# Performance work log

Measured on AMD Instinct MI355X. Metric: run time of the kernel, lower is better.

## Reference

```python
import jax, jax.numpy as jnp
import numpy as np

VOCAB, EMB, B, L, H, OUT = 100000, 300, 2048, 200, 128, 20

def setup_inputs() -> dict:
    key = jax.random.key(0)
    ks = jax.random.split(key, 7)
    x = jax.random.randint(ks[0], (B, L), 0, VOCAB, dtype=jnp.int64 if jax.config.read('jax_enable_x64') else jnp.int32)
    lengths = jax.random.randint(ks[1], (B,), 1, L + 1, dtype=x.dtype)  # avoid zero length
    emb_table = jax.random.normal(ks[2], (VOCAB, EMB), dtype=jnp.float32)
    W1 = jax.random.normal(ks[3], (EMB, H), dtype=jnp.float32) * (1.0 / np.sqrt(EMB))
    b1 = jax.random.normal(ks[4], (H,), dtype=jnp.float32) * 0.01
    W2 = jax.random.normal(ks[5], (H, OUT), dtype=jnp.float32) * (1.0 / np.sqrt(H))
    b2 = jax.random.normal(ks[6], (OUT,), dtype=jnp.float32) * 0.01
    return {"x": x, "lengths": lengths, "emb_table": emb_table,
            "W1": W1, "b1": b1, "W2": W2, "b2": b2}

def reference(x, lengths, emb_table, W1, b1, W2, b2):
    # embedding lookup: [B, L, EMB]
    emb = emb_table[x]
    # faithful to original: sum over FULL sequence, divide by per-sample length
    rep = emb.sum(axis=1) / lengths.astype(emb.dtype)[:, None]  # [B, EMB]
    h = jax.nn.relu(rep @ W1 + b1)                              # [B, H]
    logits = h @ W2 + b2                                        # [B, OUT]
    return logits
```

## Files before the change

kernel.cpp:

```cpp
#include <hip/hip_runtime.h>

#define BB   2048
#define LL   200
#define EMB  300
#define HH   128
#define OUTD 20
#define NSRT 256
#define RPW  (LL / 4)

__global__ __launch_bounds__(256) void fused_dnn(
    const int*   __restrict__ x,
    const int*   __restrict__ lengths,
    const float* __restrict__ table,
    const float* __restrict__ W1,
    const float* __restrict__ b1,
    const float* __restrict__ W2,
    const float* __restrict__ b2,
    float*       __restrict__ out)
{
    __shared__ int    idx_s[NSRT];
    __shared__ float4 part_s[4][76];
    __shared__ float  rep_s[EMB];
    __shared__ float  h_part[2][HH];
    __shared__ float  h_s[HH];

    const int b    = blockIdx.x;
    const int t    = threadIdx.x;
    const int w    = t >> 6;
    const int lane = t & 63;

    idx_s[t] = (t < LL) ? x[b * LL + t] : 0x7FFFFFFF;
    __syncthreads();

    #pragma unroll
    for (int k = 2; k <= NSRT; k <<= 1) {
        #pragma unroll
        for (int j = k >> 1; j > 0; j >>= 1) {
            const int ixj = t ^ j;
            if (ixj > t) {
                const int a0 = idx_s[t];
                const int a1 = idx_s[ixj];
                const bool up = ((t & k) == 0);
                if ((a0 > a1) == up) { idx_s[t] = a1; idx_s[ixj] = a0; }
            }
            __syncthreads();
        }
    }

    const int myidx = (lane < RPW) ? idx_s[w + 4 * lane] : 0;

    float4 acc_a = make_float4(0.f, 0.f, 0.f, 0.f);
    float4 acc_b = make_float4(0.f, 0.f, 0.f, 0.f);
    const bool hasb = (lane < (EMB / 4 - 64));

    #pragma unroll 5
    for (int i = 0; i < RPW; ++i) {
        const int ridx = __builtin_amdgcn_readlane(myidx, i);
        const float4* row = (const float4*)(table + (size_t)ridx * EMB);
        float4 va = row[lane];
        acc_a.x += va.x; acc_a.y += va.y; acc_a.z += va.z; acc_a.w += va.w;
        if (hasb) {
            float4 vb = row[64 + lane];
            acc_b.x += vb.x; acc_b.y += vb.y; acc_b.z += vb.z; acc_b.w += vb.w;
        }
    }

    part_s[w][lane] = acc_a;
    if (hasb) part_s[w][64 + lane] = acc_b;
    __syncthreads();

    const float inv_len = 1.0f / (float)lengths[b];
    const float* ps = (const float*)part_s;
    {
        float s = ps[t] + ps[304 + t] + ps[608 + t] + ps[912 + t];
        rep_s[t] = s * inv_len;
    }
    if (t < (EMB - 256)) {
        int c = 256 + t;
        float s = ps[c] + ps[304 + c] + ps[608 + c] + ps[912 + c];
        rep_s[c] = s * inv_len;
    }
    __syncthreads();

    {
        const int half = t >> 7;
        const int col  = t & 127;
        float hacc = (half == 0) ? b1[col] : 0.0f;
        const int k0 = half * (EMB / 2);
        #pragma unroll 5
        for (int k = k0; k < k0 + EMB / 2; ++k)
            hacc = fmaf(rep_s[k], W1[k * HH + col], hacc);
        h_part[half][col] = hacc;
    }
    __syncthreads();
    if (t < HH)
        h_s[t] = fmaxf(h_part[0][t] + h_part[1][t], 0.0f);
    __syncthreads();

    if (t < OUTD) {
        float oacc = b2[t];
        #pragma unroll
        for (int k = 0; k < HH; ++k)
            oacc = fmaf(h_s[k], W2[k * OUTD + t], oacc);
        out[b * OUTD + t] = oacc;
    }
}

extern "C" void kernel_launch(void* const* d_in, const int* in_sizes, int n_in,
                              void* d_out, int out_size, void* d_ws, size_t ws_size,
                              hipStream_t stream) {
    const int*   x       = (const int*)  d_in[0];
    const int*   lengths = (const int*)  d_in[1];
    const float* table   = (const float*)d_in[2];
    const float* W1      = (const float*)d_in[3];
    const float* b1      = (const float*)d_in[4];
    const float* W2      = (const float*)d_in[5];
    const float* b2      = (const float*)d_in[6];
    float*       out     = (float*)d_out;

    fused_dnn<<<BB, 256, 0, stream>>>(x, lengths, table, W1, b1, W2, b2, out);
}
```

Measured before the change: 241.6 us.

## Software-pipeline embedding row gathers and repack tail columns across lanes

The main gather loop now keeps a rolling buffer of six row loads in flight, so several independent global loads are outstanding per wave instead of one at a time. The 11 leftover float4 columns per row used to be handled by a predicated second load on 11 of 64 lanes. They are now spread across 55 lanes, each covering 5 row subsets, and gathered in a separate double-buffered pass. This raises memory-level parallelism and lane utilisation for the tail. In exchange it costs more registers, an extra shared buffer, and a 20-term reduction for the tail columns.

```diff
diff --git a/kernel.cpp b/kernel.cpp
--- a/kernel.cpp
+++ b/kernel.cpp
@@ -7,6 +7,7 @@
 #define OUTD 20
 #define NSRT 256
 #define RPW  (LL / 4)
+#define DP   6
 
 __global__ __launch_bounds__(256) void fused_dnn(
     const int*   __restrict__ x,
@@ -19,7 +20,8 @@
     float*       __restrict__ out)
 {
     __shared__ int    idx_s[NSRT];
-    __shared__ float4 part_s[4][76];
+    __shared__ float4 part_s[4][64];
+    __shared__ float4 tails[4][56];
     __shared__ float  rep_s[EMB];
     __shared__ float  h_part[2][HH];
     __shared__ float  h_s[HH];
@@ -50,35 +52,66 @@
     const int myidx = (lane < RPW) ? idx_s[w + 4 * lane] : 0;
 
     float4 acc_a = make_float4(0.f, 0.f, 0.f, 0.f);
-    float4 acc_b = make_float4(0.f, 0.f, 0.f, 0.f);
-    const bool hasb = (lane < (EMB / 4 - 64));
-
-    #pragma unroll 5
-    for (int i = 0; i < RPW; ++i) {
-        const int ridx = __builtin_amdgcn_readlane(myidx, i);
-        const float4* row = (const float4*)(table + (size_t)ridx * EMB);
-        float4 va = row[lane];
-        acc_a.x += va.x; acc_a.y += va.y; acc_a.z += va.z; acc_a.w += va.w;
-        if (hasb) {
-            float4 vb = row[64 + lane];
-            acc_b.x += vb.x; acc_b.y += vb.y; acc_b.z += vb.z; acc_b.w += vb.w;
+    {
+        float4 buf[DP];
+        #pragma unroll
+        for (int u = 0; u < DP; ++u) {
+            const int r = __builtin_amdgcn_readlane(myidx, u);
+            buf[u] = ((const float4*)(table + (size_t)r * EMB))[lane];
+        }
+        #pragma unroll
+        for (int i = 0; i < RPW; ++i) {
+            const float4 v = buf[i % DP];
+            if (i + DP < RPW) {
+                const int r = __builtin_amdgcn_readlane(myidx, i + DP);
+                buf[i % DP] = ((const float4*)(table + (size_t)r * EMB))[lane];
+            }
+            acc_a.x += v.x; acc_a.y += v.y; acc_a.z += v.z; acc_a.w += v.w;
         }
     }
+    part_s[w][lane] = acc_a;
 
-    part_s[w][lane] = acc_a;
-    if (hasb) part_s[w][64 + lane] = acc_b;
+    float4 acc_t = make_float4(0.f, 0.f, 0.f, 0.f);
+    {
+        const int g     = lane % 11;
+        const int sub   = lane / 11;
+        const int sub_c = (lane < 55) ? sub : 4;
+        float4 tbuf[2];
+        #pragma unroll
+        for (int u = 0; u < 2; ++u) {
+            const int r = idx_s[w + 4 * (u * 5 + sub_c)];
+            tbuf[u] = ((const float4*)(table + (size_t)r * EMB))[64 + g];
+        }
+        #pragma unroll
+        for (int i = 0; i < RPW / 5; ++i) {
+            const float4 v = tbuf[i & 1];
+            if (i + 2 < RPW / 5) {
+                const int r = idx_s[w + 4 * ((i + 2) * 5 + sub_c)];
+                tbuf[i & 1] = ((const float4*)(table + (size_t)r * EMB))[64 + g];
+            }
+            acc_t.x += v.x; acc_t.y += v.y; acc_t.z += v.z; acc_t.w += v.w;
+        }
+        tails[w][sub_c * 11 + g] = acc_t;
+    }
     __syncthreads();
 
     const float inv_len = 1.0f / (float)lengths[b];
-    const float* ps = (const float*)part_s;
     {
-        float s = ps[t] + ps[304 + t] + ps[608 + t] + ps[912 + t];
+        const float* ps = (const float*)part_s;
+        float s = ps[t] + ps[256 + t] + ps[512 + t] + ps[768 + t];
         rep_s[t] = s * inv_len;
     }
     if (t < (EMB - 256)) {
-        int c = 256 + t;
-        float s = ps[c] + ps[304 + c] + ps[608 + c] + ps[912 + c];
-        rep_s[c] = s * inv_len;
+        const int g4   = t >> 2;
+        const int comp = t & 3;
+        const float* tf = (const float*)tails;
+        float s = 0.f;
+        #pragma unroll
+        for (int ww = 0; ww < 4; ++ww)
+            #pragma unroll
+            for (int sb = 0; sb < 5; ++sb)
+                s += tf[(ww * 56 + sb * 11 + g4) * 4 + comp];
+        rep_s[256 + t] = s * inv_len;
     }
     __syncthreads();
 
```

Measured after the change: 244.6 us. No clear change (+1.3%).

## Quantize embedding table to int8 per row before gathering

Applied to the files above, without the earlier changes.

Adds a pre-pass kernel that quantizes the full fp32 embedding table into int8 with a per-row scale, stored in workspace. The fused kernel then gathers 300-byte int8 rows and dequantizes them with an FMA, instead of gathering 1200-byte fp32 rows. The aim is to cut the random-gather traffic, which dominates the cost, at the price of a full streaming pass over the table on every call and lossy quantization error in the sums. It falls back to the fp32 path when the workspace is too small.

```diff
diff --git a/kernel.cpp b/kernel.cpp
--- a/kernel.cpp
+++ b/kernel.cpp
@@ -1,14 +1,166 @@
 #include <hip/hip_runtime.h>
 
-#define BB   2048
-#define LL   200
-#define EMB  300
-#define HH   128
-#define OUTD 20
-#define NSRT 256
-#define RPW  (LL / 4)
-
-__global__ __launch_bounds__(256) void fused_dnn(
+#define BB    2048
+#define LL    200
+#define EMB   300
+#define HH    128
+#define OUTD  20
+#define NSRT  256
+#define VOCAB 100000
+#define RPW   (LL / 4)
+
+#define QTAB_BYTES (VOCAB * 300)
+#define SC_OFF     QTAB_BYTES
+#define WS_NEED    (QTAB_BYTES + VOCAB * 4)
+
+__global__ __launch_bounds__(256) void quant_table(
+    const float*   __restrict__ table,
+    unsigned char* __restrict__ qt,
+    float*         __restrict__ sc)
+{
+    const int row  = blockIdx.x * 4 + (threadIdx.x >> 6);
+    const int lane = threadIdx.x & 63;
+    const bool hb  = (lane < (EMB / 4 - 64));
+
+    const float4* rp = (const float4*)(table + (size_t)row * EMB);
+    float4 fa = rp[lane];
+    float4 fb = make_float4(0.f, 0.f, 0.f, 0.f);
+    if (hb) fb = rp[64 + lane];
+
+    float m = fmaxf(fmaxf(fabsf(fa.x), fabsf(fa.y)), fmaxf(fabsf(fa.z), fabsf(fa.w)));
+    m = fmaxf(m, fmaxf(fmaxf(fabsf(fb.x), fabsf(fb.y)), fmaxf(fabsf(fb.z), fabsf(fb.w))));
+    #pragma unroll
+    for (int o = 32; o >= 1; o >>= 1)
+        m = fmaxf(m, __shfl_xor(m, o, 64));
+
+    const float inv   = (m > 0.f) ? 127.0f / m : 0.0f;
+    const float scale = (m > 0.f) ? m / 127.0f : 0.0f;
+
+    unsigned int* qrow = (unsigned int*)(qt + (size_t)row * 300);
+    {
+        const unsigned int q0 = (unsigned int)((int)rintf(fa.x * inv) & 0xff);
+        const unsigned int q1 = (unsigned int)((int)rintf(fa.y * inv) & 0xff);
+        const unsigned int q2 = (unsigned int)((int)rintf(fa.z * inv) & 0xff);
+        const unsigned int q3 = (unsigned int)((int)rintf(fa.w * inv) & 0xff);
+        qrow[lane] = q0 | (q1 << 8) | (q2 << 16) | (q3 << 24);
+    }
+    if (hb) {
+        const unsigned int q0 = (unsigned int)((int)rintf(fb.x * inv) & 0xff);
+        const unsigned int q1 = (unsigned int)((int)rintf(fb.y * inv) & 0xff);
+        const unsigned int q2 = (unsigned int)((int)rintf(fb.z * inv) & 0xff);
+        const unsigned int q3 = (unsigned int)((int)rintf(fb.w * inv) & 0xff);
+        qrow[64 + lane] = q0 | (q1 << 8) | (q2 << 16) | (q3 << 24);
+    }
+    if (lane == 0) sc[row] = scale;
+}
+
+__global__ __launch_bounds__(256) void fused_dnn_q8(
+    const int*           __restrict__ x,
+    const int*           __restrict__ lengths,
+    const unsigned char* __restrict__ qt,
+    const float*         __restrict__ sc,
+    const float*         __restrict__ W1,
+    const float*         __restrict__ b1,
+    const float*         __restrict__ W2,
+    const float*         __restrict__ b2,
+    float*               __restrict__ out)
+{
+    __shared__ int    idx_s[NSRT];
+    __shared__ float4 part_s[4][76];
+    __shared__ float  rep_s[EMB];
+    __shared__ float  h_part[2][HH];
+    __shared__ float  h_s[HH];
+
+    const int b    = blockIdx.x;
+    const int t    = threadIdx.x;
+    const int w    = t >> 6;
+    const int lane = t & 63;
+
+    idx_s[t] = (t < LL) ? x[b * LL + t] : 0x7FFFFFFF;
+    __syncthreads();
+
+    #pragma unroll
+    for (int k = 2; k <= NSRT; k <<= 1) {
+        #pragma unroll
+        for (int j = k >> 1; j > 0; j >>= 1) {
+            const int ixj = t ^ j;
+            if (ixj > t) {
+                const int a0 = idx_s[t];
+                const int a1 = idx_s[ixj];
+                const bool up = ((t & k) == 0);
+                if ((a0 > a1) == up) { idx_s[t] = a1; idx_s[ixj] = a0; }
+            }
+            __syncthreads();
+        }
+    }
+
+    const int myidx = (lane < RPW) ? idx_s[w + 4 * lane] : 0;
+
+    float4 acc_a = make_float4(0.f, 0.f, 0.f, 0.f);
+    float4 acc_b = make_float4(0.f, 0.f, 0.f, 0.f);
+    const bool hasb = (lane < (EMB / 4 - 64));
+
+    #pragma unroll 4
+    for (int i = 0; i < RPW; ++i) {
+        const int ridx = __builtin_amdgcn_readlane(myidx, i);
+        const unsigned int* qrow = (const unsigned int*)(qt + (size_t)ridx * 300);
+        const float s = sc[ridx];
+        const unsigned int ua = qrow[lane];
+        acc_a.x = fmaf(s, (float)(signed char)(ua      ), acc_a.x);
+        acc_a.y = fmaf(s, (float)(signed char)(ua >>  8), acc_a.y);
+        acc_a.z = fmaf(s, (float)(signed char)(ua >> 16), acc_a.z);
+        acc_a.w = fmaf(s, (float)(signed char)(ua >> 24), acc_a.w);
+        if (hasb) {
+            const unsigned int ub = qrow[64 + lane];
+            acc_b.x = fmaf(s, (float)(signed char)(ub      ), acc_b.x);
+            acc_b.y = fmaf(s, (float)(signed char)(ub >>  8), acc_b.y);
+            acc_b.z = fmaf(s, (float)(signed char)(ub >> 16), acc_b.z);
+            acc_b.w = fmaf(s, (float)(signed char)(ub >> 24), acc_b.w);
+        }
+    }
+
+    part_s[w][lane] = acc_a;
+    if (hasb) part_s[w][64 + lane] = acc_b;
+    __syncthreads();
+
+    const float inv_len = 1.0f / (float)lengths[b];
+    const float* ps = (const float*)part_s;
+    {
+        float sv = ps[t] + ps[304 + t] + ps[608 + t] + ps[912 + t];
+        rep_s[t] = sv * inv_len;
+    }
+    if (t < (EMB - 256)) {
+        int c = 256 + t;
+        float sv = ps[c] + ps[304 + c] + ps[608 + c] + ps[912 + c];
+        rep_s[c] = sv * inv_len;
+    }
+    __syncthreads();
+
+    {
+        const int half = t >> 7;
+        const int col  = t & 127;
+        float hacc = (half == 0) ? b1[col] : 0.0f;
+        const int k0 = half * (EMB / 2);
+        #pragma unroll 5
+        for (int k = k0; k < k0 + EMB / 2; ++k)
+            hacc = fmaf(rep_s[k], W1[k * HH + col], hacc);
+        h_part[half][col] = hacc;
+    }
+    __syncthreads();
+    if (t < HH)
+        h_s[t] = fmaxf(h_part[0][t] + h_part[1][t], 0.0f);
+    __syncthreads();
+
+    if (t < OUTD) {
+        float oacc = b2[t];
+        #pragma unroll
+        for (int k = 0; k < HH; ++k)
+            oacc = fmaf(h_s[k], W2[k * OUTD + t], oacc);
+        out[b * OUTD + t] = oacc;
+    }
+}
+
+__global__ __launch_bounds__(256) void fused_dnn_f32(
     const int*   __restrict__ x,
     const int*   __restrict__ lengths,
     const float* __restrict__ table,
@@ -72,13 +224,13 @@
     const float inv_len = 1.0f / (float)lengths[b];
     const float* ps = (const float*)part_s;
     {
-        float s = ps[t] + ps[304 + t] + ps[608 + t] + ps[912 + t];
-        rep_s[t] = s * inv_len;
+        float sv = ps[t] + ps[304 + t] + ps[608 + t] + ps[912 + t];
+        rep_s[t] = sv * inv_len;
     }
     if (t < (EMB - 256)) {
         int c = 256 + t;
-        float s = ps[c] + ps[304 + c] + ps[608 + c] + ps[912 + c];
-        rep_s[c] = s * inv_len;
+        float sv = ps[c] + ps[304 + c] + ps[608 + c] + ps[912 + c];
+        rep_s[c] = sv * inv_len;
     }
     __syncthreads();
 
@@ -118,5 +270,12 @@
     const float* b2      = (const float*)d_in[6];
     float*       out     = (float*)d_out;
 
-    fused_dnn<<<BB, 256, 0, stream>>>(x, lengths, table, W1, b1, W2, b2, out);
-}
+    if (ws_size >= (size_t)WS_NEED) {
+        unsigned char* qt = (unsigned char*)d_ws;
+        float*         sc = (float*)((char*)d_ws + SC_OFF);
+        quant_table<<<VOCAB / 4, 256, 0, stream>>>(table, qt, sc);
+        fused_dnn_q8<<<BB, 256, 0, stream>>>(x, lengths, qt, sc, W1, b1, W2, b2, out);
+    } else {
+        fused_dnn_f32<<<BB, 256, 0, stream>>>(x, lengths, table, W1, b1, W2, b2, out);
+    }
+}
```

Result: slower. 266.9 us (+10.4%).

## Pre-project embedding table through W1 with MFMA and gather int8 rows

Applied to the files above, without the earlier changes.

Reorders the maths so the whole embedding table is multiplied by W1 first, using bf16 MFMA in a new kernel, rather than projecting after pooling. The projected rows are quantized to int8 with a per-row scale and stored in workspace. The per-sample kernel then gathers 128-byte int8 rows instead of 1200-byte fp32 rows, cutting gather traffic sharply. In exchange it adds a full-table read and a GEMM on every call, and it loses precision through bf16 inputs and int8 storage. The old fp32 kernel remains as a fallback when the workspace is too small.

```diff
diff --git a/kernel.cpp b/kernel.cpp
--- a/kernel.cpp
+++ b/kernel.cpp
@@ -1,33 +1,185 @@
 #include <hip/hip_runtime.h>
 
-#define BB   2048
-#define LL   200
-#define EMB  300
-#define HH   128
-#define OUTD 20
-#define NSRT 256
-#define RPW  (LL / 4)
-
-__global__ __launch_bounds__(256) void fused_dnn(
-    const int*   __restrict__ x,
-    const int*   __restrict__ lengths,
+#define BB    2048
+#define LL    200
+#define EMB   300
+#define HH    128
+#define OUTD  20
+#define NSRT  256
+#define VOCAB 100000
+#define RPW   (LL / 4)
+
+#define QT_BYTES ((size_t)VOCAB * HH)
+#define SC_OFF   QT_BYTES
+#define WS_NEED  (QT_BYTES + (size_t)VOCAB * 4)
+
+typedef short  bf16x8 __attribute__((ext_vector_type(8)));
+typedef float  f32x4  __attribute__((ext_vector_type(4)));
+
+__device__ __forceinline__ unsigned short f2bf(float x) {
+    unsigned int u = __float_as_uint(x);
+    return (unsigned short)((u + 0x7fffu + ((u >> 16) & 1u)) >> 16);
+}
+
+__global__ __launch_bounds__(256) void proj_quant(
     const float* __restrict__ table,
     const float* __restrict__ W1,
-    const float* __restrict__ b1,
-    const float* __restrict__ W2,
-    const float* __restrict__ b2,
-    float*       __restrict__ out)
+    unsigned char* __restrict__ qt,
+    float* __restrict__ sc)
 {
-    __shared__ int    idx_s[NSRT];
-    __shared__ float4 part_s[4][76];
-    __shared__ float  rep_s[EMB];
-    __shared__ float  h_part[2][HH];
-    __shared__ float  h_s[HH];
-
-    const int b    = blockIdx.x;
+    __shared__ __align__(16) unsigned char bstage[40960];
+
     const int t    = threadIdx.x;
     const int w    = t >> 6;
     const int lane = t & 63;
+    const int quad = lane >> 4;
+    const int c16  = lane & 15;
+    const int m_base = blockIdx.x * 256 + w * 64;
+
+    f32x4 acc[4][8];
+    #pragma unroll
+    for (int mt = 0; mt < 4; ++mt)
+        #pragma unroll
+        for (int nt = 0; nt < 8; ++nt)
+            acc[mt][nt] = (f32x4){0.f, 0.f, 0.f, 0.f};
+
+    #pragma unroll
+    for (int ph = 0; ph < 2; ++ph) {
+        __syncthreads();
+        #pragma unroll
+        for (int i = 0; i < 10; ++i) {
+            const int s   = t + 256 * i;
+            const int ktl = s >> 9;
+            const int rem = s & 511;
+            const int nt  = rem >> 6;
+            const int ls  = rem & 63;
+            const int q   = ls >> 4;
+            const int n   = nt * 16 + (ls & 15);
+            const int k0  = (ph * 5 + ktl) * 32 + q * 8;
+            unsigned int pk[4];
+            #pragma unroll
+            for (int jj = 0; jj < 4; ++jj) {
+                const int ka = k0 + 2 * jj, kb = ka + 1;
+                const float f0 = (ka < EMB) ? W1[ka * HH + n] : 0.f;
+                const float f1 = (kb < EMB) ? W1[kb * HH + n] : 0.f;
+                pk[jj] = (unsigned int)f2bf(f0) | ((unsigned int)f2bf(f1) << 16);
+            }
+            *(uint4*)(bstage + (size_t)s * 16) = make_uint4(pk[0], pk[1], pk[2], pk[3]);
+        }
+        __syncthreads();
+
+        #pragma unroll
+        for (int ktl = 0; ktl < 5; ++ktl) {
+            const int kt = ph * 5 + ktl;
+            bf16x8 bf[8];
+            #pragma unroll
+            for (int nt = 0; nt < 8; ++nt)
+                bf[nt] = *(const bf16x8*)(bstage + ((ktl * 8 + nt) * 64 + lane) * 16);
+
+            #pragma unroll
+            for (int mt = 0; mt < 4; ++mt) {
+                int row = m_base + mt * 16 + c16;
+                if (row > VOCAB - 1) row = VOCAB - 1;
+                const float* base = table + (size_t)row * EMB;
+                const int k0 = kt * 32 + quad * 8;
+                float f[8];
+                if (k0 + 8 <= EMB) {
+                    float4 a = *(const float4*)(base + k0);
+                    float4 b = *(const float4*)(base + k0 + 4);
+                    f[0]=a.x; f[1]=a.y; f[2]=a.z; f[3]=a.w;
+                    f[4]=b.x; f[5]=b.y; f[6]=b.z; f[7]=b.w;
+                } else if (k0 < EMB) {
+                    float4 a = *(const float4*)(base + k0);
+                    f[0]=a.x; f[1]=a.y; f[2]=a.z; f[3]=a.w;
+                    f[4]=0.f; f[5]=0.f; f[6]=0.f; f[7]=0.f;
+                } else {
+                    #pragma unroll
+                    for (int jj = 0; jj < 8; ++jj) f[jj] = 0.f;
+                }
+                bf16x8 af;
+                #pragma unroll
+                for (int jj = 0; jj < 8; ++jj) af[jj] = (short)f2bf(f[jj]);
+
+                #pragma unroll
+                for (int nt = 0; nt < 8; ++nt)
+                    acc[mt][nt] = __builtin_amdgcn_mfma_f32_16x16x32_bf16(
+                        af, bf[nt], acc[mt][nt], 0, 0, 0);
+            }
+        }
+    }
+
+    __syncthreads();
+    unsigned char* st = bstage + w * 8192;
+
+    #pragma unroll
+    for (int mt = 0; mt < 4; ++mt) {
+        float mx[4];
+        #pragma unroll
+        for (int r = 0; r < 4; ++r) {
+            float m = 0.f;
+            #pragma unroll
+            for (int nt = 0; nt < 8; ++nt) m = fmaxf(m, fabsf(acc[mt][nt][r]));
+            mx[r] = m;
+        }
+        #pragma unroll
+        for (int o = 1; o < 16; o <<= 1)
+            #pragma unroll
+            for (int r = 0; r < 4; ++r)
+                mx[r] = fmaxf(mx[r], __shfl_xor(mx[r], o, 64));
+
+        float inv[4], scl[4];
+        #pragma unroll
+        for (int r = 0; r < 4; ++r) {
+            scl[r] = mx[r] * (1.0f / 127.0f);
+            inv[r] = (mx[r] > 0.f) ? 127.0f / mx[r] : 0.f;
+        }
+        #pragma unroll
+        for (int r = 0; r < 4; ++r)
+            #pragma unroll
+            for (int nt = 0; nt < 8; ++nt) {
+                const int q = (int)rintf(acc[mt][nt][r] * inv[r]);
+                st[(mt * 16 + quad * 4 + r) * 128 + nt * 16 + c16] =
+                    (unsigned char)(q & 0xff);
+            }
+        if (c16 == 0) {
+            #pragma unroll
+            for (int r = 0; r < 4; ++r) {
+                const int grow = m_base + mt * 16 + quad * 4 + r;
+                if (grow < VOCAB) sc[grow] = scl[r];
+            }
+        }
+    }
+    __syncthreads();
+    #pragma unroll
+    for (int i = 0; i < 8; ++i) {
+        const int idx = i * 64 + lane;
+        const int row = idx >> 3;
+        const int p   = idx & 7;
+        const int grow = m_base + row;
+        const uint4 v = *(const uint4*)(st + row * 128 + p * 16);
+        if (grow < VOCAB)
+            *(uint4*)(qt + (size_t)grow * HH + p * 16) = v;
+    }
+}
+
+__global__ __launch_bounds__(256) void fused_gather_q8(
+    const int*           __restrict__ x,
+    const int*           __restrict__ lengths,
+    const unsigned char* __restrict__ qt,
+    const float*         __restrict__ sc,
+    const float*         __restrict__ b1,
+    const float*         __restrict__ W2,
+    const float*         __restrict__ b2,
+    float*               __restrict__ out)
+{
+    __shared__ int   idx_s[NSRT];
+    __shared__ float part_f[32 * HH];
+    __shared__ float h_s[HH];
+
+    const int b = blockIdx.x;
+    const int t = threadIdx.x;
+    const int w = t >> 6;
+    const int l = t & 63;
 
     idx_s[t] = (t < LL) ? x[b * LL + t] : 0x7FFFFFFF;
     __syncthreads();
@@ -47,12 +199,98 @@
         }
     }
 
+    const int g = l >> 3;
+    const int p = l & 7;
+
+    float4 a0 = make_float4(0.f,0.f,0.f,0.f);
+    float4 a1 = make_float4(0.f,0.f,0.f,0.f);
+    float4 a2 = make_float4(0.f,0.f,0.f,0.f);
+    float4 a3 = make_float4(0.f,0.f,0.f,0.f);
+
+    #pragma unroll
+    for (int i = 0; i < 7; ++i) {
+        const int j  = 8 * i + g;
+        const int jc = (j < RPW) ? j : (RPW - 1);
+        const int ridx = idx_s[w + 4 * jc];
+        const uint4 d = *(const uint4*)(qt + (size_t)ridx * HH + (p << 4));
+        const float sv = (j < RPW) ? sc[ridx] : 0.f;
+
+        a0.x = fmaf(sv, (float)(signed char)(d.x       ), a0.x);
+        a0.y = fmaf(sv, (float)(signed char)(d.x >>  8 ), a0.y);
+        a0.z = fmaf(sv, (float)(signed char)(d.x >> 16 ), a0.z);
+        a0.w = fmaf(sv, (float)(signed char)(d.x >> 24 ), a0.w);
+        a1.x = fmaf(sv, (float)(signed char)(d.y       ), a1.x);
+        a1.y = fmaf(sv, (float)(signed char)(d.y >>  8 ), a1.y);
+        a1.z = fmaf(sv, (float)(signed char)(d.y >> 16 ), a1.z);
+        a1.w = fmaf(sv, (float)(signed char)(d.y >> 24 ), a1.w);
+        a2.x = fmaf(sv, (float)(signed char)(d.z       ), a2.x);
+        a2.y = fmaf(sv, (float)(signed char)(d.z >>  8 ), a2.y);
+        a2.z = fmaf(sv, (float)(signed char)(d.z >> 16 ), a2.z);
+        a2.w = fmaf(sv, (float)(signed char)(d.z >> 24 ), a2.w);
+        a3.x = fmaf(sv, (float)(signed char)(d.w       ), a3.x);
+        a3.y = fmaf(sv, (float)(signed char)(d.w >>  8 ), a3.y);
+        a3.z = fmaf(sv, (float)(signed char)(d.w >> 16 ), a3.z);
+        a3.w = fmaf(sv, (float)(signed char)(d.w >> 24 ), a3.w);
+    }
+
+    {
+        float* dst = &part_f[(w * 8 + g) * HH + p * 16];
+        *(float4*)(dst + 0)  = a0;
+        *(float4*)(dst + 4)  = a1;
+        *(float4*)(dst + 8)  = a2;
+        *(float4*)(dst + 12) = a3;
+    }
+    __syncthreads();
+
+    const float inv_len = 1.0f / (float)lengths[b];
+    if (t < HH) {
+        float s = 0.f;
+        #pragma unroll
+        for (int q = 0; q < 32; ++q) s += part_f[q * HH + t];
+        h_s[t] = fmaxf(fmaf(s, inv_len, b1[t]), 0.f);
+    }
+    __syncthreads();
+
+    if (t < OUTD) {
+        float oacc = b2[t];
+        #pragma unroll
+        for (int k = 0; k < HH; ++k)
+            oacc = fmaf(h_s[k], W2[k * OUTD + t], oacc);
+        out[b * OUTD + t] = oacc;
+    }
+}
+
+__global__ __launch_bounds__(256) void fused_dnn_f32(
+    const int* __restrict__ x, const int* __restrict__ lengths,
+    const float* __restrict__ table, const float* __restrict__ W1,
+    const float* __restrict__ b1, const float* __restrict__ W2,
+    const float* __restrict__ b2, float* __restrict__ out)
+{
+    __shared__ int    idx_s[NSRT];
+    __shared__ float4 part_s[4][76];
+    __shared__ float  rep_s[EMB];
+    __shared__ float  h_part[2][HH];
+    __shared__ float  h_s[HH];
+
+    const int b = blockIdx.x, t = threadIdx.x, w = t >> 6, lane = t & 63;
+    idx_s[t] = (t < LL) ? x[b * LL + t] : 0x7FFFFFFF;
+    __syncthreads();
+    #pragma unroll
+    for (int k = 2; k <= NSRT; k <<= 1)
+        #pragma unroll
+        for (int j = k >> 1; j > 0; j >>= 1) {
+            const int ixj = t ^ j;
+            if (ixj > t) {
+                const int q0 = idx_s[t], q1 = idx_s[ixj];
+                const bool up = ((t & k) == 0);
+                if ((q0 > q1) == up) { idx_s[t] = q1; idx_s[ixj] = q0; }
+            }
+            __syncthreads();
+        }
     const int myidx = (lane < RPW) ? idx_s[w + 4 * lane] : 0;
-
-    float4 acc_a = make_float4(0.f, 0.f, 0.f, 0.f);
-    float4 acc_b = make_float4(0.f, 0.f, 0.f, 0.f);
+    float4 acc_a = make_float4(0.f,0.f,0.f,0.f);
+    float4 acc_b = make_float4(0.f,0.f,0.f,0.f);
     const bool hasb = (lane < (EMB / 4 - 64));
-
     #pragma unroll 5
     for (int i = 0; i < RPW; ++i) {
         const int ridx = __builtin_amdgcn_readlane(myidx, i);
@@ -64,46 +302,25 @@
             acc_b.x += vb.x; acc_b.y += vb.y; acc_b.z += vb.z; acc_b.w += vb.w;
         }
     }
-
     part_s[w][lane] = acc_a;
     if (hasb) part_s[w][64 + lane] = acc_b;
     __syncthreads();
-
     const float inv_len = 1.0f / (float)lengths[b];
     const float* ps = (const float*)part_s;
-    {
-        float s = ps[t] + ps[304 + t] + ps[608 + t] + ps[912 + t];
-        rep_s[t] = s * inv_len;
-    }
-    if (t < (EMB - 256)) {
-        int c = 256 + t;
-        float s = ps[c] + ps[304 + c] + ps[608 + c] + ps[912 + c];
-        rep_s[c] = s * inv_len;
-    }
-    __syncthreads();
-
-    {
-        const int half = t >> 7;
-        const int col  = t & 127;
-        float hacc = (half == 0) ? b1[col] : 0.0f;
-        const int k0 = half * (EMB / 2);
-        #pragma unroll 5
-        for (int k = k0; k < k0 + EMB / 2; ++k)
-            hacc = fmaf(rep_s[k], W1[k * HH + col], hacc);
-        h_part[half][col] = hacc;
-    }
-    __syncthreads();
-    if (t < HH)
-        h_s[t] = fmaxf(h_part[0][t] + h_part[1][t], 0.0f);
-    __syncthreads();
-
-    if (t < OUTD) {
-        float oacc = b2[t];
-        #pragma unroll
-        for (int k = 0; k < HH; ++k)
-            oacc = fmaf(h_s[k], W2[k * OUTD + t], oacc);
-        out[b * OUTD + t] = oacc;
-    }
+    { float sv = ps[t]+ps[304+t]+ps[608+t]+ps[912+t]; rep_s[t] = sv*inv_len; }
+    if (t < (EMB-256)) { int c=256+t; float sv=ps[c]+ps[304+c]+ps[608+c]+ps[912+c]; rep_s[c]=sv*inv_len; }
+    __syncthreads();
+    { const int half=t>>7, col=t&127; float hacc=(half==0)?b1[col]:0.f; const int k0=half*(EMB/2);
+      #pragma unroll 5
+      for (int k=k0;k<k0+EMB/2;++k) hacc=fmaf(rep_s[k],W1[k*HH+col],hacc);
+      h_part[half][col]=hacc; }
+    __syncthreads();
+    if (t<HH) h_s[t]=fmaxf(h_part[0][t]+h_part[1][t],0.f);
+    __syncthreads();
+    if (t<OUTD) { float o=b2[t];
+        #pragma unroll
+        for (int k=0;k<HH;++k) o=fmaf(h_s[k],W2[k*OUTD+t],o);
+        out[b*OUTD+t]=o; }
 }
 
 extern "C" void kernel_launch(void* const* d_in, const int* in_sizes, int n_in,
@@ -118,5 +335,12 @@
     const float* b2      = (const float*)d_in[6];
     float*       out     = (float*)d_out;
 
-    fused_dnn<<<BB, 256, 0, stream>>>(x, lengths, table, W1, b1, W2, b2, out);
-}
+    if (ws_size >= WS_NEED) {
+        unsigned char* qt = (unsigned char*)d_ws;
+        float*         sc = (float*)((char*)d_ws + SC_OFF);
+        proj_quant<<<(VOCAB + 255) / 256, 256, 0, stream>>>(table, W1, qt, sc);
+        fused_gather_q8<<<BB, 256, 0, stream>>>(x, lengths, qt, sc, b1, W2, b2, out);
+    } else {
+        fused_dnn_f32<<<BB, 256, 0, stream>>>(x, lengths, table, W1, b1, W2, b2, out);
+    }
+}
```

New measurement: 247.4 us. +2.4%, slower.
